# Kernel optimization log

Measured on AMD Instinct MI355X. Metric: run time of the kernel, lower is better.

Reference implementation:

```python
import jax, jax.numpy as jnp
import numpy as np

G = 7          # num_grid
SG = 12        # size_grid = 84 // 7
A = 18         # predicted_action_space
B = 8192


def _patches(x):
    # x: [B,1,84,84] -> [B, G*G, SG*SG], patch order (i rows, j cols) matching slice_grid loop
    b = x.shape[0]
    x = x.reshape(b, G, SG, G, SG)
    return x.transpose(0, 1, 3, 2, 4).reshape(b, G * G, SG * SG)


def setup_inputs() -> dict:
    key = jax.random.key(0)
    ks = jax.random.split(key, 10)
    last_states = jax.random.uniform(ks[0], (B, 1, 84, 84), jnp.float32) * 255.0
    now_states = jax.random.uniform(ks[1], (B, 1, 84, 84), jnp.float32) * 255.0
    def w(k, shape):
        return jax.random.normal(k, shape, jnp.float32) * 0.05
    return {
        "last_states": last_states,
        "now_states": now_states,
        # mlp_e: 288 -> 256 -> 128 -> 18
        "We1": w(ks[2], (2 * SG * SG, 256)), "be1": jnp.zeros((256,), jnp.float32),
        "We2": w(ks[3], (256, 128)),          "be2": jnp.zeros((128,), jnp.float32),
        "We3": w(ks[4], (128, A)),            "be3": jnp.zeros((A,), jnp.float32),
        # mlp_alpha: 144 -> 64 -> 64 -> 1
        "Wa1": w(ks[5], (SG * SG, 64)), "ba1": jnp.zeros((64,), jnp.float32),
        "Wa2": w(ks[6], (64, 64)),       "ba2": jnp.zeros((64,), jnp.float32),
        "Wa3": w(ks[7], (64, 1)),        "ba3": jnp.zeros((1,), jnp.float32),
    }


def reference(last_states, now_states, We1, be1, We2, be2, We3, be3,
              Wa1, ba1, Wa2, ba2, Wa3, ba3):
    last = last_states / 255.0
    now = now_states / 255.0
    p_now = _patches(now)            # [B, P, 144]
    p_last = _patches(last)          # [B, P, 144]

    # alpha: per-patch scalar via small MLP, softmax over patches
    h = jax.nn.relu(jnp.einsum('bpf,fo->bpo', p_now, Wa1) + ba1)
    h = jax.nn.relu(jnp.einsum('bpf,fo->bpo', h, Wa2) + ba2)
    alpha_logits = (jnp.einsum('bpf,fo->bpo', h, Wa3) + ba3)[..., 0]   # [B, P]
    alpha = jax.nn.softmax(alpha_logits, axis=1)

    # e: per-patch action logits from [diff, now]
    e_in = jnp.concatenate([p_now - p_last, p_now], axis=-1)           # [B, P, 288]
    g = jax.nn.relu(jnp.einsum('bpf,fo->bpo', e_in, We1) + be1)
    g = jax.nn.relu(jnp.einsum('bpf,fo->bpo', g, We2) + be2)
    e = jnp.einsum('bpf,fo->bpo', g, We3) + be3                        # [B, P, A]

    predicted_action_log_probs = jax.nn.log_softmax(
        (e * alpha[..., None]).sum(axis=1), axis=1)                    # [B, A]
    predicted_action_log_probs_each = jax.nn.log_softmax(e, axis=2)    # [B, P, A]
    loss_ent = (alpha * jnp.log(alpha)).sum(axis=1).mean()
    return predicted_action_log_probs, loss_ent, predicted_action_log_probs_each
```

## Files before the change

kernel.cpp:

```cpp
#include <hip/hip_runtime.h>
#include <math.h>

#define NPCH 49
#define NA 18
#define NB 8192
#define TOTAL (NB*NPCH)

typedef __attribute__((ext_vector_type(8))) short bf16x8;
typedef __attribute__((ext_vector_type(4))) float f32x4;

__device__ __forceinline__ unsigned short f2bf(float f) {
    unsigned int u = __float_as_uint(f);
    return (unsigned short)((u + 0x7FFFu + ((u >> 16) & 1u)) >> 16);
}

#define MF(a,b,c) __builtin_amdgcn_mfma_f32_16x16x32_bf16((a),(b),(c),0,0,0)
#define RAWBAR() do { \
    asm volatile("s_waitcnt lgkmcnt(0)" ::: "memory"); \
    __builtin_amdgcn_s_barrier(); \
    asm volatile("" ::: "memory"); \
} while (0)

#define WS_US (256*512)

__global__ __launch_bounds__(256)
void prep_weights(const float* __restrict__ We1, const float* __restrict__ We2,
                  const float* __restrict__ We3, const float* __restrict__ Wa1,
                  const float* __restrict__ Wa2, unsigned short* __restrict__ wst)
{
    int i = blockIdx.x * 256 + threadIdx.x;
    if (i >= WS_US) return;
    const int fs = i >> 9, l = (i >> 3) & 63, j = i & 7;
    const int kh = ((l >> 4) << 3) + j;
    const int nl = l & 15;
    float v = 0.0f;
    if (fs < 20) {
        int s = fs >> 2, w = fs & 3;
        int k = s * 32 + kh, n = w * 16 + nl;
        v = (k < 144) ? Wa1[k * 64 + n] : 0.0f;
    } else if (fs < 28) {
        int q = fs - 20, s = q >> 2, w = q & 3;
        v = Wa2[(s * 32 + kh) * 64 + (w * 16 + nl)];
    } else if (fs < 32) {
        v = 0.0f;
    } else if (fs < 176) {
        int q = fs - 32, s = q >> 4, nt = (q >> 2) & 3, w = q & 3;
        v = We1[(s * 32 + kh) * 256 + (w * 64 + nt * 16 + nl)];
    } else if (fs < 240) {
        int q = fs - 176, s = q >> 3, nt = (q >> 2) & 1, w = q & 3;
        v = We2[(s * 32 + kh) * 128 + (w * 32 + nt * 16 + nl)];
    } else if (fs < 248) {
        int q = fs - 240, s = q >> 1, nt = q & 1;
        int n = nt * 16 + nl;
        v = (n < NA) ? We3[(s * 32 + kh) * NA + n] : 0.0f;
    }
    wst[i] = f2bf(v);
}

__device__ __forceinline__ void wb_frag(unsigned short* base, f32x4 a)
{
    float r0 = fmaxf(a[0], 0.f), r1 = fmaxf(a[1], 0.f);
    float r2 = fmaxf(a[2], 0.f), r3 = fmaxf(a[3], 0.f);
    unsigned u01, u23;
    asm("v_cvt_pk_bf16_f32 %0, %1, %2" : "=v"(u01) : "v"(r0), "v"(r1));
    asm("v_cvt_pk_bf16_f32 %0, %1, %2" : "=v"(u23) : "v"(r2), "v"(r3));
    base[0]  = (unsigned short)u01;
    base[8]  = (unsigned short)(u01 >> 16);
    base[16] = (unsigned short)u23;
    base[24] = (unsigned short)(u23 >> 16);
}

__global__ __launch_bounds__(256, 3)
void fused_mfma_kernel(const float* __restrict__ last_s, const float* __restrict__ now_s,
                       const unsigned short* __restrict__ wstream,
                       const float* __restrict__ be1, const float* __restrict__ be2,
                       const float* __restrict__ be3, const float* __restrict__ ba1,
                       const float* __restrict__ ba2, const float* __restrict__ ba3,
                       const float* __restrict__ Wa3,
                       float* __restrict__ out_each, float* __restrict__ out_probs,
                       float* __restrict__ ws_ent)
{
    __shared__ __align__(16) unsigned char smem[46080];
    unsigned short* Ein = (unsigned short*)smem;
    unsigned short* H1  = (unsigned short*)smem;
    unsigned short* H2  = (unsigned short*)smem;
    unsigned short* HA1 = (unsigned short*)(smem + 36864);
    float*          APT = (float*)(smem + 45056);
    float*          ALG = (float*)(smem + 36864);
    float*          OE  = (float*)(smem + 37120);

    const int t    = threadIdx.x;
    const int lane = t & 63;
    const int wid  = t >> 6;
    const int g    = lane >> 4;
    const int rl   = lane & 15;
    const int img  = blockIdx.x;

#define GFRAG(fs) (*(const bf16x8*)(wstream + (size_t)(fs) * 512 + lane * 8))

    bf16x8 wa1f[5], wa2f[2];
    #pragma unroll
    for (int s = 0; s < 5; ++s) wa1f[s] = GFRAG(s * 4 + wid);
    #pragma unroll
    for (int s = 0; s < 2; ++s) wa2f[s] = GFRAG(20 + s * 4 + wid);
    bf16x8 wA[4], wB[4], wC[4];
    #pragma unroll
    for (int nt = 0; nt < 4; ++nt) wA[nt] = GFRAG(32 + 0 * 16 + nt * 4 + wid);
    #pragma unroll
    for (int nt = 0; nt < 4; ++nt) wB[nt] = GFRAG(32 + 1 * 16 + nt * 4 + wid);
    #pragma unroll
    for (int nt = 0; nt < 4; ++nt) wC[nt] = GFRAG(32 + 2 * 16 + nt * 4 + wid);

    {
        const float* nowI  = now_s  + (size_t)img * 7056;
        const float* lastI = last_s + (size_t)img * 7056;
        #pragma unroll
        for (int it = 0; it < 7; ++it) {
            const int i = t + it * 256;
            if (i < 1764) {
                const float4 n4 = *(const float4*)(nowI + i * 4);
                const float4 l4 = *(const float4*)(lastI + i * 4);
                const int px = i * 4, row = px / 84, col = px - row * 84;
                const int pi = row / 12, fr = row - pi * 12;
                const int pj = col / 12, fc = col - pj * 12;
                const int p = pi * 7 + pj, f = fr * 12 + fc;
                const int wp = p >> 4, rp = p & 15;
                const float k255 = 1.0f / 255.0f;
                float d0 = (n4.x - l4.x) * k255, d1 = (n4.y - l4.y) * k255;
                float d2 = (n4.z - l4.z) * k255, d3 = (n4.w - l4.w) * k255;
                float w0 = n4.x * k255, w1 = n4.y * k255;
                float w2 = n4.z * k255, w3 = n4.w * k255;
                unsigned da, db, wa, wb;
                asm("v_cvt_pk_bf16_f32 %0, %1, %2" : "=v"(da) : "v"(d0), "v"(d1));
                asm("v_cvt_pk_bf16_f32 %0, %1, %2" : "=v"(db) : "v"(d2), "v"(d3));
                asm("v_cvt_pk_bf16_f32 %0, %1, %2" : "=v"(wa) : "v"(w0), "v"(w1));
                asm("v_cvt_pk_bf16_f32 %0, %1, %2" : "=v"(wb) : "v"(w2), "v"(w3));
                const int s1 = f >> 5, g1 = (f >> 3) & 3, j1 = f & 7;
                *(uint2*)(Ein + (wp * 9 + s1) * 512 + g1 * 128 + rp * 8 + j1) = (uint2){da, db};
                const int k2 = 144 + f;
                const int s2 = k2 >> 5, g2 = (k2 >> 3) & 3, j2 = k2 & 7;
                *(uint2*)(Ein + (wp * 9 + s2) * 512 + g2 * 128 + rp * 8 + j2) = (uint2){wa, wb};
            }
        }
    }
    RAWBAR();

    const int colA = wid * 16 + rl;
    {
        const float b1 = ba1[colA];
        f32x4 accA[4];
        #pragma unroll
        for (int mt = 0; mt < 4; ++mt) accA[mt] = (f32x4){b1, b1, b1, b1};
        #pragma unroll
        for (int sa = 0; sa < 5; ++sa) {
            int ok = 144 + sa * 32 + g * 8;
            if (ok > 280) ok = 280;
            #pragma unroll
            for (int mt = 0; mt < 4; ++mt) {
                const bf16x8 af = *(const bf16x8*)(Ein + (mt * 9 + (ok >> 5)) * 512 +
                                                   ((ok >> 3) & 3) * 128 + rl * 8);
                accA[mt] = MF(af, wa1f[sa], accA[mt]);
            }
        }
        const int sA  = wid >> 1;
        const int hiA = (wid & 1) * 2 + (rl >> 3);
        const int jA  = rl & 7;
        #pragma unroll
        for (int mt = 0; mt < 4; ++mt)
            wb_frag(HA1 + (mt * 2 + sA) * 512 + hiA * 128 + g * 32 + jA, accA[mt]);
    }
    RAWBAR();

    {
        const float b2 = ba2[colA];
        const float w3 = Wa3[colA];
        f32x4 accB[4];
        #pragma unroll
        for (int mt = 0; mt < 4; ++mt) accB[mt] = (f32x4){b2, b2, b2, b2};
        #pragma unroll
        for (int s = 0; s < 2; ++s) {
            #pragma unroll
            for (int mt = 0; mt < 4; ++mt) {
                const bf16x8 af = *(const bf16x8*)(HA1 + (mt * 2 + s) * 512 + lane * 8);
                accB[mt] = MF(af, wa2f[s], accB[mt]);
            }
        }
        #pragma unroll
        for (int mt = 0; mt < 4; ++mt) {
            #pragma unroll
            for (int r = 0; r < 4; ++r) {
                float v = fmaxf(accB[mt][r], 0.0f) * w3;
                v += __shfl_xor(v, 1); v += __shfl_xor(v, 2);
                v += __shfl_xor(v, 4); v += __shfl_xor(v, 8);
                if (rl == 0) APT[wid * 64 + mt * 16 + g * 4 + r] = v;
            }
        }
    }
    RAWBAR();
    if (t < NPCH)
        ALG[t] = APT[t] + APT[64 + t] + APT[128 + t] + APT[192 + t] + ba3[0];

    f32x4 acc1[4][4];
    #pragma unroll
    for (int nt = 0; nt < 4; ++nt) {
        const float b = be1[wid * 64 + nt * 16 + rl];
        #pragma unroll
        for (int mt = 0; mt < 4; ++mt) acc1[mt][nt] = (f32x4){b, b, b, b};
    }

#define E1_STEP(W, s, sn) do { \
    const bf16x8 x0_ = *(const bf16x8*)(Ein + (0 * 9 + (s)) * 512 + lane * 8); \
    const bf16x8 x1_ = *(const bf16x8*)(Ein + (1 * 9 + (s)) * 512 + lane * 8); \
    const bf16x8 x2_ = *(const bf16x8*)(Ein + (2 * 9 + (s)) * 512 + lane * 8); \
    const bf16x8 x3_ = *(const bf16x8*)(Ein + (3 * 9 + (s)) * 512 + lane * 8); \
    _Pragma("unroll") \
    for (int nt = 0; nt < 4; ++nt) { \
        acc1[0][nt] = MF(x0_, W[nt], acc1[0][nt]); \
        acc1[1][nt] = MF(x1_, W[nt], acc1[1][nt]); \
        acc1[2][nt] = MF(x2_, W[nt], acc1[2][nt]); \
        acc1[3][nt] = MF(x3_, W[nt], acc1[3][nt]); \
    } \
    if ((sn) <= 8) { \
        _Pragma("unroll") \
        for (int nt = 0; nt < 4; ++nt) W[nt] = GFRAG(32 + (sn) * 16 + nt * 4 + wid); \
    } \
} while (0)

    E1_STEP(wA, 0, 3); E1_STEP(wB, 1, 4); E1_STEP(wC, 2, 5);
    E1_STEP(wA, 3, 6); E1_STEP(wB, 4, 7); E1_STEP(wC, 5, 8);
    E1_STEP(wA, 6, 9); E1_STEP(wB, 7, 9); E1_STEP(wC, 8, 9);
#undef E1_STEP

    RAWBAR();

    #pragma unroll
    for (int mt = 0; mt < 4; ++mt) {
        #pragma unroll
        for (int nt = 0; nt < 4; ++nt) {
            const int col = wid * 64 + nt * 16 + rl;
            wb_frag(H1 + (mt * 8 + (col >> 5)) * 512 + ((col >> 3) & 3) * 128 +
                    g * 32 + (col & 7), acc1[mt][nt]);
        }
    }
    RAWBAR();

    f32x4 acc2[4][2];
    #pragma unroll
    for (int nt = 0; nt < 2; ++nt) {
        const float b = be2[wid * 32 + nt * 16 + rl];
        #pragma unroll
        for (int mt = 0; mt < 4; ++mt) acc2[mt][nt] = (f32x4){b, b, b, b};
    }
    bf16x8 vA[2], vB[2], vC[2];
    #pragma unroll
    for (int nt = 0; nt < 2; ++nt) vA[nt] = GFRAG(176 + 0 * 8 + nt * 4 + wid);
    #pragma unroll
    for (int nt = 0; nt < 2; ++nt) vB[nt] = GFRAG(176 + 1 * 8 + nt * 4 + wid);
    #pragma unroll
    for (int nt = 0; nt < 2; ++nt) vC[nt] = GFRAG(176 + 2 * 8 + nt * 4 + wid);

#define E2_STEP(V, s2, sn) do { \
    const bf16x8 x0_ = *(const bf16x8*)(H1 + (0 * 8 + (s2)) * 512 + lane * 8); \
    const bf16x8 x1_ = *(const bf16x8*)(H1 + (1 * 8 + (s2)) * 512 + lane * 8); \
    const bf16x8 x2_ = *(const bf16x8*)(H1 + (2 * 8 + (s2)) * 512 + lane * 8); \
    const bf16x8 x3_ = *(const bf16x8*)(H1 + (3 * 8 + (s2)) * 512 + lane * 8); \
    _Pragma("unroll") \
    for (int nt = 0; nt < 2; ++nt) { \
        acc2[0][nt] = MF(x0_, V[nt], acc2[0][nt]); \
        acc2[1][nt] = MF(x1_, V[nt], acc2[1][nt]); \
        acc2[2][nt] = MF(x2_, V[nt], acc2[2][nt]); \
        acc2[3][nt] = MF(x3_, V[nt], acc2[3][nt]); \
    } \
    if ((sn) <= 7) { \
        _Pragma("unroll") \
        for (int nt = 0; nt < 2; ++nt) V[nt] = GFRAG(176 + (sn) * 8 + nt * 4 + wid); \
    } \
} while (0)

    E2_STEP(vA, 0, 3); E2_STEP(vB, 1, 4); E2_STEP(vC, 2, 5);
    E2_STEP(vA, 3, 6); E2_STEP(vB, 4, 7); E2_STEP(vC, 5, 8);
    E2_STEP(vA, 6, 8); E2_STEP(vB, 7, 8);
#undef E2_STEP

    bf16x8 w3f[8];
    #pragma unroll
    for (int q = 0; q < 8; ++q) w3f[q] = GFRAG(240 + q);

    RAWBAR();

    #pragma unroll
    for (int mt = 0; mt < 4; ++mt) {
        #pragma unroll
        for (int nt = 0; nt < 2; ++nt) {
            const int c2 = nt * 16 + rl;
            wb_frag(H2 + (mt * 4 + wid) * 512 + ((c2 >> 3) & 3) * 128 +
                    g * 32 + (c2 & 7), acc2[mt][nt]);
        }
    }
    RAWBAR();

    {
        f32x4 acc3[2];
        #pragma unroll
        for (int nt = 0; nt < 2; ++nt) {
            const int col = nt * 16 + rl;
            const float b = (col < NA) ? be3[col] : 0.0f;
            acc3[nt] = (f32x4){b, b, b, b};
        }
        #pragma unroll
        for (int s = 0; s < 4; ++s) {
            const bf16x8 af = *(const bf16x8*)(H2 + (wid * 4 + s) * 512 + lane * 8);
            acc3[0] = MF(af, w3f[s * 2 + 0], acc3[0]);
            acc3[1] = MF(af, w3f[s * 2 + 1], acc3[1]);
        }
        const bool v1 = (rl < 2);
        #pragma unroll
        for (int r = 0; r < 4; ++r) {
            const int p3 = wid * 16 + g * 4 + r;
            float x0 = acc3[0][r];
            float x1 = acc3[1][r];
            float m = fmaxf(x0, v1 ? x1 : -3.0e38f);
            m = fmaxf(m, __shfl_xor(m, 1)); m = fmaxf(m, __shfl_xor(m, 2));
            m = fmaxf(m, __shfl_xor(m, 4)); m = fmaxf(m, __shfl_xor(m, 8));
            float sm = expf(x0 - m) + (v1 ? expf(x1 - m) : 0.0f);
            sm += __shfl_xor(sm, 1); sm += __shfl_xor(sm, 2);
            sm += __shfl_xor(sm, 4); sm += __shfl_xor(sm, 8);
            const float L = m + logf(sm);
            if (p3 < NPCH) {
                float* o = out_each + (size_t)(img * NPCH + p3) * NA;
                const float y0 = x0 - L;
                o[rl] = y0;
                OE[p3 * NA + rl] = y0;
                if (v1) {
                    const float y1 = x1 - L;
                    o[16 + rl] = y1;
                    OE[p3 * NA + 16 + rl] = y1;
                }
            }
        }
    }
    RAWBAR();

    if (wid == 0) {
        float lg = (lane < NPCH) ? ALG[lane] : -3.0e38f;
        float m = lg;
        #pragma unroll
        for (int off = 32; off > 0; off >>= 1) m = fmaxf(m, __shfl_xor(m, off, 64));
        float ex = (lane < NPCH) ? expf(lg - m) : 0.0f;
        float s = ex;
        #pragma unroll
        for (int off = 32; off > 0; off >>= 1) s += __shfl_xor(s, off, 64);
        const float ls = logf(s);
        const float alpha = ex / s;

        float ent = (lane < NPCH) ? alpha * (lg - m - ls) : 0.0f;
        #pragma unroll
        for (int off = 32; off > 0; off >>= 1) ent += __shfl_xor(ent, off, 64);
        if (lane == 0) ws_ent[img] = ent;

        float acc = 0.0f;
        for (int p = 0; p < NPCH; ++p) {
            const float ap = __shfl(alpha, p, 64);
            if (lane < NA) acc += ap * OE[p * NA + lane];
        }
        float mm = (lane < NA) ? acc : -3.0e38f;
        #pragma unroll
        for (int off = 32; off > 0; off >>= 1) mm = fmaxf(mm, __shfl_xor(mm, off, 64));
        float ee = (lane < NA) ? expf(acc - mm) : 0.0f;
        #pragma unroll
        for (int off = 32; off > 0; off >>= 1) ee += __shfl_xor(ee, off, 64);
        if (lane < NA) out_probs[img * NA + lane] = acc - mm - logf(ee);
    }
#undef GFRAG
}

__global__ __launch_bounds__(256)
void ent_reduce_kernel(const float* __restrict__ ws_ent, float* __restrict__ out_scalar)
{
    float s = 0.0f;
    for (int i = threadIdx.x; i < NB; i += 256) s += ws_ent[i];
    #pragma unroll
    for (int off = 32; off > 0; off >>= 1) s += __shfl_xor(s, off, 64);
    __shared__ float ps[4];
    if ((threadIdx.x & 63) == 0) ps[threadIdx.x >> 6] = s;
    __syncthreads();
    if (threadIdx.x == 0)
        out_scalar[0] = (ps[0] + ps[1] + ps[2] + ps[3]) * (1.0f / NB);
}

extern "C" void kernel_launch(void* const* d_in, const int* in_sizes, int n_in,
                              void* d_out, int out_size, void* d_ws, size_t ws_size,
                              hipStream_t stream)
{
    (void)in_sizes; (void)n_in; (void)out_size; (void)ws_size;

    const float* last_s = (const float*)d_in[0];
    const float* now_s  = (const float*)d_in[1];
    const float* We1 = (const float*)d_in[2];  const float* be1 = (const float*)d_in[3];
    const float* We2 = (const float*)d_in[4];  const float* be2 = (const float*)d_in[5];
    const float* We3 = (const float*)d_in[6];  const float* be3 = (const float*)d_in[7];
    const float* Wa1 = (const float*)d_in[8];  const float* ba1 = (const float*)d_in[9];
    const float* Wa2 = (const float*)d_in[10]; const float* ba2 = (const float*)d_in[11];
    const float* Wa3 = (const float*)d_in[12]; const float* ba3 = (const float*)d_in[13];

    float* out = (float*)d_out;
    float* out_probs = out;
    float* out_ent   = out + NB * NA;
    float* out_each  = out + NB * NA + 1;

    float* ws_ent = (float*)d_ws;
    unsigned short* wst = (unsigned short*)(ws_ent + NB);

    prep_weights<<<dim3((WS_US + 255) / 256), dim3(256), 0, stream>>>(
        We1, We2, We3, Wa1, Wa2, wst);

    fused_mfma_kernel<<<dim3(NB), dim3(256), 0, stream>>>(
        last_s, now_s, wst, be1, be2, be3, ba1, ba2, ba3, Wa3,
        out_each, out_probs, ws_ent);

    ent_reduce_kernel<<<dim3(1), dim3(256), 0, stream>>>(ws_ent, out_ent);
}
```

Before: 255.0 us.

## Interleave alpha MLP into e1 GEMM and distribute alpha-weighted reduction across waves

Moves the alpha layer-2 MFMA and reduction into the middle of the e1 GEMM steps, which removes two block barriers and lets that work overlap with the e1 pipeline. The layer-2 weight fragment loads are issued earlier, before the barrier. Each wave now computes alpha from the logits and accumulates the alpha-weighted log-probs in registers, writing per-wave partial sums to shared memory. This replaces the serial single-wave 49-step loop over the OE buffer. The cost is more register pressure and some redundant exp/softmax work repeated in every wave.

Result: no change. 256.4 us (+0.5%).

```diff
diff --git a/kernel.cpp b/kernel.cpp
--- a/kernel.cpp
+++ b/kernel.cpp
@@ -87,7 +87,7 @@
     unsigned short* HA1 = (unsigned short*)(smem + 36864);
     float*          APT = (float*)(smem + 45056);
     float*          ALG = (float*)(smem + 36864);
-    float*          OE  = (float*)(smem + 37120);
+    float*          PSUM= (float*)(smem + 45056);
 
     const int t    = threadIdx.x;
     const int lane = t & 63;
@@ -169,36 +169,6 @@
         for (int mt = 0; mt < 4; ++mt)
             wb_frag(HA1 + (mt * 2 + sA) * 512 + hiA * 128 + g * 32 + jA, accA[mt]);
     }
-    RAWBAR();
-
-    {
-        const float b2 = ba2[colA];
-        const float w3 = Wa3[colA];
-        f32x4 accB[4];
-        #pragma unroll
-        for (int mt = 0; mt < 4; ++mt) accB[mt] = (f32x4){b2, b2, b2, b2};
-        #pragma unroll
-        for (int s = 0; s < 2; ++s) {
-            #pragma unroll
-            for (int mt = 0; mt < 4; ++mt) {
-                const bf16x8 af = *(const bf16x8*)(HA1 + (mt * 2 + s) * 512 + lane * 8);
-                accB[mt] = MF(af, wa2f[s], accB[mt]);
-            }
-        }
-        #pragma unroll
-        for (int mt = 0; mt < 4; ++mt) {
-            #pragma unroll
-            for (int r = 0; r < 4; ++r) {
-                float v = fmaxf(accB[mt][r], 0.0f) * w3;
-                v += __shfl_xor(v, 1); v += __shfl_xor(v, 2);
-                v += __shfl_xor(v, 4); v += __shfl_xor(v, 8);
-                if (rl == 0) APT[wid * 64 + mt * 16 + g * 4 + r] = v;
-            }
-        }
-    }
-    RAWBAR();
-    if (t < NPCH)
-        ALG[t] = APT[t] + APT[64 + t] + APT[128 + t] + APT[192 + t] + ba3[0];
 
     f32x4 acc1[4][4];
     #pragma unroll
@@ -227,11 +197,51 @@
 } while (0)
 
     E1_STEP(wA, 0, 3); E1_STEP(wB, 1, 4); E1_STEP(wC, 2, 5);
-    E1_STEP(wA, 3, 6); E1_STEP(wB, 4, 7); E1_STEP(wC, 5, 8);
-    E1_STEP(wA, 6, 9); E1_STEP(wB, 7, 9); E1_STEP(wC, 8, 9);
+    E1_STEP(wA, 3, 6); E1_STEP(wB, 4, 7);
+
+    RAWBAR();
+
+    {
+        const float b2 = ba2[colA];
+        const float w3 = Wa3[colA];
+        f32x4 accB[4];
+        #pragma unroll
+        for (int mt = 0; mt < 4; ++mt) accB[mt] = (f32x4){b2, b2, b2, b2};
+        #pragma unroll
+        for (int s = 0; s < 2; ++s) {
+            #pragma unroll
+            for (int mt = 0; mt < 4; ++mt) {
+                const bf16x8 af = *(const bf16x8*)(HA1 + (mt * 2 + s) * 512 + lane * 8);
+                accB[mt] = MF(af, wa2f[s], accB[mt]);
+            }
+        }
+        #pragma unroll
+        for (int mt = 0; mt < 4; ++mt) {
+            #pragma unroll
+            for (int r = 0; r < 4; ++r) {
+                float v = fmaxf(accB[mt][r], 0.0f) * w3;
+                v += __shfl_xor(v, 1); v += __shfl_xor(v, 2);
+                v += __shfl_xor(v, 4); v += __shfl_xor(v, 8);
+                if (rl == 0) APT[wid * 64 + mt * 16 + g * 4 + r] = v;
+            }
+        }
+    }
+
+    E1_STEP(wC, 5, 8); E1_STEP(wA, 6, 9); E1_STEP(wB, 7, 9); E1_STEP(wC, 8, 9);
 #undef E1_STEP
 
-    RAWBAR();
+    bf16x8 vA[2], vB[2], vC[2];
+    #pragma unroll
+    for (int nt = 0; nt < 2; ++nt) vA[nt] = GFRAG(176 + 0 * 8 + nt * 4 + wid);
+    #pragma unroll
+    for (int nt = 0; nt < 2; ++nt) vB[nt] = GFRAG(176 + 1 * 8 + nt * 4 + wid);
+    #pragma unroll
+    for (int nt = 0; nt < 2; ++nt) vC[nt] = GFRAG(176 + 2 * 8 + nt * 4 + wid);
+
+    RAWBAR();
+
+    if (t < NPCH)
+        ALG[t] = APT[t] + APT[64 + t] + APT[128 + t] + APT[192 + t] + ba3[0];
 
     #pragma unroll
     for (int mt = 0; mt < 4; ++mt) {
@@ -251,13 +261,6 @@
         #pragma unroll
         for (int mt = 0; mt < 4; ++mt) acc2[mt][nt] = (f32x4){b, b, b, b};
     }
-    bf16x8 vA[2], vB[2], vC[2];
-    #pragma unroll
-    for (int nt = 0; nt < 2; ++nt) vA[nt] = GFRAG(176 + 0 * 8 + nt * 4 + wid);
-    #pragma unroll
-    for (int nt = 0; nt < 2; ++nt) vB[nt] = GFRAG(176 + 1 * 8 + nt * 4 + wid);
-    #pragma unroll
-    for (int nt = 0; nt < 2; ++nt) vC[nt] = GFRAG(176 + 2 * 8 + nt * 4 + wid);
 
 #define E2_STEP(V, s2, sn) do { \
     const bf16x8 x0_ = *(const bf16x8*)(H1 + (0 * 8 + (s2)) * 512 + lane * 8); \
@@ -300,6 +303,16 @@
     RAWBAR();
 
     {
+        float lg = (lane < NPCH) ? ALG[lane] : -3.0e38f;
+        float am = lg;
+        #pragma unroll
+        for (int off = 32; off > 0; off >>= 1) am = fmaxf(am, __shfl_xor(am, off, 64));
+        float aex = (lane < NPCH) ? expf(lg - am) : 0.0f;
+        float ase = aex;
+        #pragma unroll
+        for (int off = 32; off > 0; off >>= 1) ase += __shfl_xor(ase, off, 64);
+        const float inv_ase = 1.0f / ase;
+
         f32x4 acc3[2];
         #pragma unroll
         for (int nt = 0; nt < 2; ++nt) {
@@ -314,9 +327,11 @@
             acc3[1] = MF(af, w3f[s * 2 + 1], acc3[1]);
         }
         const bool v1 = (rl < 2);
+        float part0 = 0.0f, part1 = 0.0f;
         #pragma unroll
         for (int r = 0; r < 4; ++r) {
             const int p3 = wid * 16 + g * 4 + r;
+            const bool valid = (p3 < NPCH);
             float x0 = acc3[0][r];
             float x1 = acc3[1][r];
             float m = fmaxf(x0, v1 ? x1 : -3.0e38f);
@@ -326,50 +341,42 @@
             sm += __shfl_xor(sm, 1); sm += __shfl_xor(sm, 2);
             sm += __shfl_xor(sm, 4); sm += __shfl_xor(sm, 8);
             const float L = m + logf(sm);
-            if (p3 < NPCH) {
+            const float y0 = x0 - L;
+            const float y1 = x1 - L;
+            const float ap = valid ? expf(ALG[p3] - am) * inv_ase : 0.0f;
+            part0 += valid ? ap * y0 : 0.0f;
+            part1 += valid ? ap * y1 : 0.0f;
+            if (valid) {
                 float* o = out_each + (size_t)(img * NPCH + p3) * NA;
-                const float y0 = x0 - L;
                 o[rl] = y0;
-                OE[p3 * NA + rl] = y0;
-                if (v1) {
-                    const float y1 = x1 - L;
-                    o[16 + rl] = y1;
-                    OE[p3 * NA + 16 + rl] = y1;
-                }
+                if (v1) o[16 + rl] = y1;
             }
         }
+        part0 += __shfl_xor(part0, 16, 64); part0 += __shfl_xor(part0, 32, 64);
+        part1 += __shfl_xor(part1, 16, 64); part1 += __shfl_xor(part1, 32, 64);
+        if (lane < 16) PSUM[wid * 18 + lane] = part0;
+        if (lane < 2)  PSUM[wid * 18 + 16 + lane] = part1;
+
+        if (wid == 0) {
+            float ent = (lane < NPCH) ? (aex * inv_ase) * (lg - am - logf(ase)) : 0.0f;
+            #pragma unroll
+            for (int off = 32; off > 0; off >>= 1) ent += __shfl_xor(ent, off, 64);
+            if (lane == 0) ws_ent[img] = ent;
+        }
     }
     RAWBAR();
 
     if (wid == 0) {
-        float lg = (lane < NPCH) ? ALG[lane] : -3.0e38f;
-        float m = lg;
-        #pragma unroll
-        for (int off = 32; off > 0; off >>= 1) m = fmaxf(m, __shfl_xor(m, off, 64));
-        float ex = (lane < NPCH) ? expf(lg - m) : 0.0f;
-        float s = ex;
-        #pragma unroll
-        for (int off = 32; off > 0; off >>= 1) s += __shfl_xor(s, off, 64);
-        const float ls = logf(s);
-        const float alpha = ex / s;
-
-        float ent = (lane < NPCH) ? alpha * (lg - m - ls) : 0.0f;
-        #pragma unroll
-        for (int off = 32; off > 0; off >>= 1) ent += __shfl_xor(ent, off, 64);
-        if (lane == 0) ws_ent[img] = ent;
-
-        float acc = 0.0f;
-        for (int p = 0; p < NPCH; ++p) {
-            const float ap = __shfl(alpha, p, 64);
-            if (lane < NA) acc += ap * OE[p * NA + lane];
-        }
-        float mm = (lane < NA) ? acc : -3.0e38f;
+        float tot = 0.0f;
+        if (lane < NA)
+            tot = PSUM[lane] + PSUM[18 + lane] + PSUM[36 + lane] + PSUM[54 + lane];
+        float mm = (lane < NA) ? tot : -3.0e38f;
         #pragma unroll
         for (int off = 32; off > 0; off >>= 1) mm = fmaxf(mm, __shfl_xor(mm, off, 64));
-        float ee = (lane < NA) ? expf(acc - mm) : 0.0f;
+        float ee = (lane < NA) ? expf(tot - mm) : 0.0f;
         #pragma unroll
         for (int off = 32; off > 0; off >>= 1) ee += __shfl_xor(ee, off, 64);
-        if (lane < NA) out_probs[img * NA + lane] = acc - mm - logf(ee);
+        if (lane < NA) out_probs[img * NA + lane] = tot - mm - logf(ee);
     }
 #undef GFRAG
 }
```

## Pack 64 patch rows per block and split alpha softmax into combine kernel

Applied to the files above, without the earlier changes.

The main kernel now handles a dense run of 64 flattened (image, patch) rows per block instead of one image with 49 patches padded to 64. This removes the wasted padding rows in every MFMA tile. The cross-patch softmax, entropy and weighted log-softmax move to a new per-image kernel, which reads alpha logits and per-patch log-probs back from global memory. The alpha second layer is interleaved into the E1 MFMA stream and weight-fragment loads are hoisted before the barrier. In exchange there is an extra launch and extra global traffic for re-reading out_each, and the gather of input patches is less coalesced.

Result: faster. 227.5 us (-10.8%).

```diff
diff --git a/kernel.cpp b/kernel.cpp
--- a/kernel.cpp
+++ b/kernel.cpp
@@ -5,6 +5,7 @@
 #define NA 18
 #define NB 8192
 #define TOTAL (NB*NPCH)
+#define NBLK (TOTAL/64)
 
 typedef __attribute__((ext_vector_type(8))) short bf16x8;
 typedef __attribute__((ext_vector_type(4))) float f32x4;
@@ -77,8 +78,7 @@
                        const float* __restrict__ be3, const float* __restrict__ ba1,
                        const float* __restrict__ ba2, const float* __restrict__ ba3,
                        const float* __restrict__ Wa3,
-                       float* __restrict__ out_each, float* __restrict__ out_probs,
-                       float* __restrict__ ws_ent)
+                       float* __restrict__ out_each, float* __restrict__ ws_alpha)
 {
     __shared__ __align__(16) unsigned char smem[46080];
     unsigned short* Ein = (unsigned short*)smem;
@@ -86,15 +86,13 @@
     unsigned short* H2  = (unsigned short*)smem;
     unsigned short* HA1 = (unsigned short*)(smem + 36864);
     float*          APT = (float*)(smem + 45056);
-    float*          ALG = (float*)(smem + 36864);
-    float*          OE  = (float*)(smem + 37120);
 
     const int t    = threadIdx.x;
     const int lane = t & 63;
     const int wid  = t >> 6;
     const int g    = lane >> 4;
     const int rl   = lane & 15;
-    const int img  = blockIdx.x;
+    const int row0 = blockIdx.x * 64;
 
 #define GFRAG(fs) (*(const bf16x8*)(wstream + (size_t)(fs) * 512 + lane * 8))
 
@@ -112,35 +110,36 @@
     for (int nt = 0; nt < 4; ++nt) wC[nt] = GFRAG(32 + 2 * 16 + nt * 4 + wid);
 
     {
-        const float* nowI  = now_s  + (size_t)img * 7056;
-        const float* lastI = last_s + (size_t)img * 7056;
-        #pragma unroll
-        for (int it = 0; it < 7; ++it) {
-            const int i = t + it * 256;
-            if (i < 1764) {
-                const float4 n4 = *(const float4*)(nowI + i * 4);
-                const float4 l4 = *(const float4*)(lastI + i * 4);
-                const int px = i * 4, row = px / 84, col = px - row * 84;
-                const int pi = row / 12, fr = row - pi * 12;
-                const int pj = col / 12, fc = col - pj * 12;
-                const int p = pi * 7 + pj, f = fr * 12 + fc;
-                const int wp = p >> 4, rp = p & 15;
-                const float k255 = 1.0f / 255.0f;
-                float d0 = (n4.x - l4.x) * k255, d1 = (n4.y - l4.y) * k255;
-                float d2 = (n4.z - l4.z) * k255, d3 = (n4.w - l4.w) * k255;
-                float w0 = n4.x * k255, w1 = n4.y * k255;
-                float w2 = n4.z * k255, w3 = n4.w * k255;
-                unsigned da, db, wa, wb;
-                asm("v_cvt_pk_bf16_f32 %0, %1, %2" : "=v"(da) : "v"(d0), "v"(d1));
-                asm("v_cvt_pk_bf16_f32 %0, %1, %2" : "=v"(db) : "v"(d2), "v"(d3));
-                asm("v_cvt_pk_bf16_f32 %0, %1, %2" : "=v"(wa) : "v"(w0), "v"(w1));
-                asm("v_cvt_pk_bf16_f32 %0, %1, %2" : "=v"(wb) : "v"(w2), "v"(w3));
-                const int s1 = f >> 5, g1 = (f >> 3) & 3, j1 = f & 7;
-                *(uint2*)(Ein + (wp * 9 + s1) * 512 + g1 * 128 + rp * 8 + j1) = (uint2){da, db};
-                const int k2 = 144 + f;
-                const int s2 = k2 >> 5, g2 = (k2 >> 3) & 3, j2 = k2 & 7;
-                *(uint2*)(Ein + (wp * 9 + s2) * 512 + g2 * 128 + rp * 8 + j2) = (uint2){wa, wb};
-            }
+        #pragma unroll
+        for (int it = 0; it < 9; ++it) {
+            const int idx = t + it * 256;
+            const int r   = idx / 36;
+            const int q   = idx - r * 36;
+            const int R   = row0 + r;
+            const int im  = R / 49;
+            const int p   = R - im * 49;
+            const int pi  = p / 7,  pj  = p - pi * 7;
+            const int fr  = q / 3,  fc4 = q - fr * 3;
+            const size_t base = (size_t)im * 7056 + (pi * 12 + fr) * 84 + pj * 12 + fc4 * 4;
+            const float4 n4 = *(const float4*)(now_s + base);
+            const float4 l4 = *(const float4*)(last_s + base);
+            const float k255 = 1.0f / 255.0f;
+            float d0 = (n4.x - l4.x) * k255, d1 = (n4.y - l4.y) * k255;
+            float d2 = (n4.z - l4.z) * k255, d3 = (n4.w - l4.w) * k255;
+            float w0 = n4.x * k255, w1 = n4.y * k255;
+            float w2 = n4.z * k255, w3 = n4.w * k255;
+            unsigned da, db, wa, wb;
+            asm("v_cvt_pk_bf16_f32 %0, %1, %2" : "=v"(da) : "v"(d0), "v"(d1));
+            asm("v_cvt_pk_bf16_f32 %0, %1, %2" : "=v"(db) : "v"(d2), "v"(d3));
+            asm("v_cvt_pk_bf16_f32 %0, %1, %2" : "=v"(wa) : "v"(w0), "v"(w1));
+            asm("v_cvt_pk_bf16_f32 %0, %1, %2" : "=v"(wb) : "v"(w2), "v"(w3));
+            const int wp = r >> 4, rp = r & 15;
+            const int f  = fr * 12 + fc4 * 4;
+            const int s1 = f >> 5, g1 = (f >> 3) & 3, j1 = f & 7;
+            *(uint2*)(Ein + (wp * 9 + s1) * 512 + g1 * 128 + rp * 8 + j1) = (uint2){da, db};
+            const int k2 = 144 + f;
+            const int s2 = k2 >> 5, g2 = (k2 >> 3) & 3, j2 = k2 & 7;
+            *(uint2*)(Ein + (wp * 9 + s2) * 512 + g2 * 128 + rp * 8 + j2) = (uint2){wa, wb};
         }
     }
     RAWBAR();
@@ -169,36 +168,6 @@
         for (int mt = 0; mt < 4; ++mt)
             wb_frag(HA1 + (mt * 2 + sA) * 512 + hiA * 128 + g * 32 + jA, accA[mt]);
     }
-    RAWBAR();
-
-    {
-        const float b2 = ba2[colA];
-        const float w3 = Wa3[colA];
-        f32x4 accB[4];
-        #pragma unroll
-        for (int mt = 0; mt < 4; ++mt) accB[mt] = (f32x4){b2, b2, b2, b2};
-        #pragma unroll
-        for (int s = 0; s < 2; ++s) {
-            #pragma unroll
-            for (int mt = 0; mt < 4; ++mt) {
-                const bf16x8 af = *(const bf16x8*)(HA1 + (mt * 2 + s) * 512 + lane * 8);
-                accB[mt] = MF(af, wa2f[s], accB[mt]);
-            }
-        }
-        #pragma unroll
-        for (int mt = 0; mt < 4; ++mt) {
-            #pragma unroll
-            for (int r = 0; r < 4; ++r) {
-                float v = fmaxf(accB[mt][r], 0.0f) * w3;
-                v += __shfl_xor(v, 1); v += __shfl_xor(v, 2);
-                v += __shfl_xor(v, 4); v += __shfl_xor(v, 8);
-                if (rl == 0) APT[wid * 64 + mt * 16 + g * 4 + r] = v;
-            }
-        }
-    }
-    RAWBAR();
-    if (t < NPCH)
-        ALG[t] = APT[t] + APT[64 + t] + APT[128 + t] + APT[192 + t] + ba3[0];
 
     f32x4 acc1[4][4];
     #pragma unroll
@@ -227,11 +196,51 @@
 } while (0)
 
     E1_STEP(wA, 0, 3); E1_STEP(wB, 1, 4); E1_STEP(wC, 2, 5);
-    E1_STEP(wA, 3, 6); E1_STEP(wB, 4, 7); E1_STEP(wC, 5, 8);
-    E1_STEP(wA, 6, 9); E1_STEP(wB, 7, 9); E1_STEP(wC, 8, 9);
+    E1_STEP(wA, 3, 6); E1_STEP(wB, 4, 7);
+
+    RAWBAR();
+
+    {
+        const float b2 = ba2[colA];
+        const float w3 = Wa3[colA];
+        f32x4 accB[4];
+        #pragma unroll
+        for (int mt = 0; mt < 4; ++mt) accB[mt] = (f32x4){b2, b2, b2, b2};
+        #pragma unroll
+        for (int s = 0; s < 2; ++s) {
+            #pragma unroll
+            for (int mt = 0; mt < 4; ++mt) {
+                const bf16x8 af = *(const bf16x8*)(HA1 + (mt * 2 + s) * 512 + lane * 8);
+                accB[mt] = MF(af, wa2f[s], accB[mt]);
+            }
+        }
+        #pragma unroll
+        for (int mt = 0; mt < 4; ++mt) {
+            #pragma unroll
+            for (int r = 0; r < 4; ++r) {
+                float v = fmaxf(accB[mt][r], 0.0f) * w3;
+                v += __shfl_xor(v, 1); v += __shfl_xor(v, 2);
+                v += __shfl_xor(v, 4); v += __shfl_xor(v, 8);
+                if (rl == 0) APT[wid * 64 + mt * 16 + g * 4 + r] = v;
+            }
+        }
+    }
+
+    E1_STEP(wC, 5, 8); E1_STEP(wA, 6, 9); E1_STEP(wB, 7, 9); E1_STEP(wC, 8, 9);
 #undef E1_STEP
 
-    RAWBAR();
+    bf16x8 vA[2], vB[2], vC[2];
+    #pragma unroll
+    for (int nt = 0; nt < 2; ++nt) vA[nt] = GFRAG(176 + 0 * 8 + nt * 4 + wid);
+    #pragma unroll
+    for (int nt = 0; nt < 2; ++nt) vB[nt] = GFRAG(176 + 1 * 8 + nt * 4 + wid);
+    #pragma unroll
+    for (int nt = 0; nt < 2; ++nt) vC[nt] = GFRAG(176 + 2 * 8 + nt * 4 + wid);
+
+    RAWBAR();
+
+    if (t < 64)
+        ws_alpha[row0 + t] = APT[t] + APT[64 + t] + APT[128 + t] + APT[192 + t] + ba3[0];
 
     #pragma unroll
     for (int mt = 0; mt < 4; ++mt) {
@@ -251,13 +260,6 @@
         #pragma unroll
         for (int mt = 0; mt < 4; ++mt) acc2[mt][nt] = (f32x4){b, b, b, b};
     }
-    bf16x8 vA[2], vB[2], vC[2];
-    #pragma unroll
-    for (int nt = 0; nt < 2; ++nt) vA[nt] = GFRAG(176 + 0 * 8 + nt * 4 + wid);
-    #pragma unroll
-    for (int nt = 0; nt < 2; ++nt) vB[nt] = GFRAG(176 + 1 * 8 + nt * 4 + wid);
-    #pragma unroll
-    for (int nt = 0; nt < 2; ++nt) vC[nt] = GFRAG(176 + 2 * 8 + nt * 4 + wid);
 
 #define E2_STEP(V, s2, sn) do { \
     const bf16x8 x0_ = *(const bf16x8*)(H1 + (0 * 8 + (s2)) * 512 + lane * 8); \
@@ -316,7 +318,7 @@
         const bool v1 = (rl < 2);
         #pragma unroll
         for (int r = 0; r < 4; ++r) {
-            const int p3 = wid * 16 + g * 4 + r;
+            const int prow = row0 + wid * 16 + g * 4 + r;
             float x0 = acc3[0][r];
             float x1 = acc3[1][r];
             float m = fmaxf(x0, v1 ? x1 : -3.0e38f);
@@ -326,52 +328,52 @@
             sm += __shfl_xor(sm, 1); sm += __shfl_xor(sm, 2);
             sm += __shfl_xor(sm, 4); sm += __shfl_xor(sm, 8);
             const float L = m + logf(sm);
-            if (p3 < NPCH) {
-                float* o = out_each + (size_t)(img * NPCH + p3) * NA;
-                const float y0 = x0 - L;
-                o[rl] = y0;
-                OE[p3 * NA + rl] = y0;
-                if (v1) {
-                    const float y1 = x1 - L;
-                    o[16 + rl] = y1;
-                    OE[p3 * NA + 16 + rl] = y1;
-                }
-            }
-        }
-    }
-    RAWBAR();
-
-    if (wid == 0) {
-        float lg = (lane < NPCH) ? ALG[lane] : -3.0e38f;
-        float m = lg;
-        #pragma unroll
-        for (int off = 32; off > 0; off >>= 1) m = fmaxf(m, __shfl_xor(m, off, 64));
-        float ex = (lane < NPCH) ? expf(lg - m) : 0.0f;
-        float s = ex;
-        #pragma unroll
-        for (int off = 32; off > 0; off >>= 1) s += __shfl_xor(s, off, 64);
-        const float ls = logf(s);
-        const float alpha = ex / s;
-
-        float ent = (lane < NPCH) ? alpha * (lg - m - ls) : 0.0f;
-        #pragma unroll
-        for (int off = 32; off > 0; off >>= 1) ent += __shfl_xor(ent, off, 64);
-        if (lane == 0) ws_ent[img] = ent;
-
-        float acc = 0.0f;
-        for (int p = 0; p < NPCH; ++p) {
-            const float ap = __shfl(alpha, p, 64);
-            if (lane < NA) acc += ap * OE[p * NA + lane];
-        }
-        float mm = (lane < NA) ? acc : -3.0e38f;
-        #pragma unroll
-        for (int off = 32; off > 0; off >>= 1) mm = fmaxf(mm, __shfl_xor(mm, off, 64));
-        float ee = (lane < NA) ? expf(acc - mm) : 0.0f;
-        #pragma unroll
-        for (int off = 32; off > 0; off >>= 1) ee += __shfl_xor(ee, off, 64);
-        if (lane < NA) out_probs[img * NA + lane] = acc - mm - logf(ee);
+            float* o = out_each + (size_t)prow * NA;
+            o[rl] = x0 - L;
+            if (v1) o[16 + rl] = x1 - L;
+        }
     }
 #undef GFRAG
+}
+
+__global__ __launch_bounds__(64)
+void alpha_combine_kernel(const float* __restrict__ ws_alpha,
+                          const float* __restrict__ out_each,
+                          float* __restrict__ out_probs,
+                          float* __restrict__ ws_ent)
+{
+    const int b = blockIdx.x;
+    const int lane = threadIdx.x;
+
+    float lg = (lane < NPCH) ? ws_alpha[b * NPCH + lane] : -3.0e38f;
+    float m = lg;
+    #pragma unroll
+    for (int off = 32; off > 0; off >>= 1) m = fmaxf(m, __shfl_xor(m, off, 64));
+    float ex = (lane < NPCH) ? expf(lg - m) : 0.0f;
+    float s = ex;
+    #pragma unroll
+    for (int off = 32; off > 0; off >>= 1) s += __shfl_xor(s, off, 64);
+    const float ls = logf(s);
+    const float alpha = ex / s;
+
+    float ent = (lane < NPCH) ? alpha * (lg - m - ls) : 0.0f;
+    #pragma unroll
+    for (int off = 32; off > 0; off >>= 1) ent += __shfl_xor(ent, off, 64);
+    if (lane == 0) ws_ent[b] = ent;
+
+    float acc = 0.0f;
+    const float* eb = out_each + (size_t)b * NPCH * NA;
+    for (int p = 0; p < NPCH; ++p) {
+        const float ap = __shfl(alpha, p, 64);
+        if (lane < NA) acc += ap * eb[p * NA + lane];
+    }
+    float mm = (lane < NA) ? acc : -3.0e38f;
+    #pragma unroll
+    for (int off = 32; off > 0; off >>= 1) mm = fmaxf(mm, __shfl_xor(mm, off, 64));
+    float ee = (lane < NA) ? expf(acc - mm) : 0.0f;
+    #pragma unroll
+    for (int off = 32; off > 0; off >>= 1) ee += __shfl_xor(ee, off, 64);
+    if (lane < NA) out_probs[b * NA + lane] = acc - mm - logf(ee);
 }
 
 __global__ __launch_bounds__(256)
@@ -408,15 +410,19 @@
     float* out_ent   = out + NB * NA;
     float* out_each  = out + NB * NA + 1;
 
-    float* ws_ent = (float*)d_ws;
+    float* ws_alpha = (float*)d_ws;
+    float* ws_ent   = ws_alpha + TOTAL;
     unsigned short* wst = (unsigned short*)(ws_ent + NB);
 
     prep_weights<<<dim3((WS_US + 255) / 256), dim3(256), 0, stream>>>(
         We1, We2, We3, Wa1, Wa2, wst);
 
-    fused_mfma_kernel<<<dim3(NB), dim3(256), 0, stream>>>(
+    fused_mfma_kernel<<<dim3(NBLK), dim3(256), 0, stream>>>(
         last_s, now_s, wst, be1, be2, be3, ba1, ba2, ba3, Wa3,
-        out_each, out_probs, ws_ent);
+        out_each, ws_alpha);
+
+    alpha_combine_kernel<<<dim3(NB), dim3(64), 0, stream>>>(
+        ws_alpha, out_each, out_probs, ws_ent);
 
     ent_reduce_kernel<<<dim3(1), dim3(256), 0, stream>>>(ws_ent, out_ent);
 }
```
